# Optimization experiments

Measured on AMD Instinct MI355X. Metric: run time of the kernel, lower is better.

## Reference

```python
import jax, jax.numpy as jnp
import numpy as np
import math

B, T, WIDTH, NUM_HEADS, WINDOW = 2, 2048, 1024, 16, 1024
HEAD_DIM = WIDTH // NUM_HEADS
_MIN_LOGITS_VALUE = -1e30


def setup_inputs() -> dict:
    key = jax.random.key(0)
    k1, k2, k3, k4, k5 = jax.random.split(key, 5)
    std = math.sqrt(1.0 / WIDTH)
    x = jax.random.normal(k1, (B, T, WIDTH), dtype=jnp.float32)
    segment_pos = jnp.tile(jnp.arange(T, dtype=jnp.int32)[None, :], (B, 1))
    Wq = jax.random.normal(k2, (WIDTH, WIDTH), dtype=jnp.float32) * std
    Wk = jax.random.normal(k3, (HEAD_DIM, WIDTH), dtype=jnp.float32) * std
    Wv = jax.random.normal(k4, (HEAD_DIM, WIDTH), dtype=jnp.float32) * std
    Wf = jax.random.normal(k5, (WIDTH, WIDTH), dtype=jnp.float32) * std
    bf = jnp.zeros((WIDTH,), dtype=jnp.float32)
    return {"x": x, "segment_pos": segment_pos, "Wq": Wq, "Wk": Wk, "Wv": Wv, "Wf": Wf, "bf": bf}


def reference(x, segment_pos, Wq, Wk, Wv, Wf, bf):
    b, t, _ = x.shape
    # projections (torch Linear: y = x @ W.T)
    q = (x @ Wq.T).reshape(b, t, NUM_HEADS, HEAD_DIM)  # b t n h
    k = x @ Wk.T  # b s h  (single shared KV head, MQA)
    v = x @ Wv.T  # b s h
    scale = 1.0 / math.sqrt(HEAD_DIM)
    logits = jnp.einsum('btnh,bsh->bnts', q, k) * scale
    pos = jnp.arange(t)
    q_pos = pos[:, None]
    k_pos = pos[None, :]
    mask = (q_pos >= k_pos) & (q_pos <= k_pos + WINDOW)  # [t, t]
    masked = jnp.where(mask[None, None, :, :], logits, _MIN_LOGITS_VALUE)
    probs = jax.nn.softmax(masked.astype(jnp.float32), axis=-1).astype(logits.dtype)
    out = jnp.einsum('bnts,bsh->btnh', probs, v).reshape(b, t, WIDTH)
    return out @ Wf.T + bf
```

## Files before the change

### kernel.cpp

```cpp
#include <hip/hip_runtime.h>
#include <cstdint>
#include <cstddef>

#define BB      2
#define TT      2048
#define WID     1024
#define NH      16
#define HD      64
#define WIN     1024
#define MROWS   (BB*TT)
#define NQKV    1152
#define QSCL    0.18033688011112042f

typedef __attribute__((ext_vector_type(8))) short  short8;
typedef __attribute__((ext_vector_type(4))) float  floatx4;

__device__ __forceinline__ unsigned short f2bf(float f) {
  union { float f; unsigned int u; } v; v.f = f;
  unsigned int u = v.u;
  unsigned int r = (u + 0x7fffu + ((u >> 16) & 1u)) >> 16;
  return (unsigned short)r;
}

__device__ __forceinline__ float fast_exp2(float x) {
#if __has_builtin(__builtin_amdgcn_exp2f)
  return __builtin_amdgcn_exp2f(x);
#else
  return exp2f(x);
#endif
}

__device__ __forceinline__ unsigned int pk_bf16_trunc(float lo, float hi) {
  union { float f; unsigned int u; } a, b; a.f = lo; b.f = hi;
#if __has_builtin(__builtin_amdgcn_perm)
  return __builtin_amdgcn_perm(b.u, a.u, 0x07060302u);
#else
  return (b.u & 0xffff0000u) | (a.u >> 16);
#endif
}

__device__ __forceinline__ void gld_lds16(const void* g, void* l) {
  __builtin_amdgcn_global_load_lds(
      (const __attribute__((address_space(1))) unsigned int*)g,
      (__attribute__((address_space(3))) unsigned int*)l, 16, 0, 0);
}

__global__ __launch_bounds__(256) void convert_kernel(
    const float* __restrict__ x,  const float* __restrict__ wq,
    const float* __restrict__ wk, const float* __restrict__ wv,
    const float* __restrict__ wf,
    unsigned short* __restrict__ xb, unsigned short* __restrict__ wb,
    unsigned short* __restrict__ wfb)
{
  const int NX4 = (MROWS * WID) / 4;
  const int NQ4 = (WID * WID) / 4;
  const int NK4 = (HD * WID) / 4;
  const int NW4 = NQ4 + 2 * NK4;
  const int NF4 = (WID * WID) / 4;
  const int TOT = NX4 + NW4 + NF4;
  for (int i = blockIdx.x * blockDim.x + threadIdx.x; i < TOT;
       i += gridDim.x * blockDim.x) {
    float4 v4;
    unsigned short* dptr;
    if (i < NX4) {
      v4 = ((const float4*)x)[i];
      dptr = xb + (size_t)i * 4;
    } else if (i < NX4 + NW4) {
      int k = i - NX4;
      dptr = wb + (size_t)k * 4;
      if (k < NQ4)            v4 = ((const float4*)wq)[k];
      else if (k < NQ4 + NK4) v4 = ((const float4*)wk)[k - NQ4];
      else                    v4 = ((const float4*)wv)[k - NQ4 - NK4];
    } else {
      int k = i - NX4 - NW4;
      v4 = ((const float4*)wf)[k];
      dptr = wfb + (size_t)k * 4;
    }
    ushort4 o4 = make_ushort4(f2bf(v4.x), f2bf(v4.y), f2bf(v4.z), f2bf(v4.w));
    *(ushort4*)dptr = o4;
  }
}

__global__ __launch_bounds__(256) void gemm64(
    const unsigned short* __restrict__ A, const unsigned short* __restrict__ Bm,
    int M, int N, int K, int mode,
    float* __restrict__ C, const float* __restrict__ bias,
    unsigned short* __restrict__ qb, unsigned short* __restrict__ kb,
    unsigned short* __restrict__ vtb)
{
  __shared__ __align__(16) unsigned short As[2][64 * 64];
  __shared__ __align__(16) unsigned short Bs[2][128 * 64];

  const int tid  = threadIdx.x;
  const int m0   = blockIdx.x * 64;
  const int n0   = blockIdx.y * 128;
  const int w    = tid >> 6;
  const int lane = tid & 63;
  const int wr   = w >> 1;
  const int wc   = w & 1;
  const int quad = lane >> 4;
  const int l16  = lane & 15;

  const int rS  = tid >> 3;
  const int cS  = tid & 7;
  const int csS = (cS + rS) & 7;
  const unsigned short* gA0 = A  + (size_t)(m0 + rS) * K + csS * 8;
  const unsigned short* gA1 = gA0 + (size_t)32 * K;
  const unsigned short* gB0 = Bm + (size_t)(n0 + rS) * K + csS * 8;
  const unsigned short* gB1 = gB0 + (size_t)32 * K;
  const unsigned short* gB2 = gB0 + (size_t)64 * K;
  const unsigned short* gB3 = gB0 + (size_t)96 * K;
  const int wub = (tid & 192) * 16;

  floatx4 acc[2][4];
#pragma unroll
  for (int it = 0; it < 2; ++it)
#pragma unroll
    for (int jt = 0; jt < 4; ++jt)
      acc[it][jt] = (floatx4){0.f, 0.f, 0.f, 0.f};

  const int K64 = K >> 6;
  gld_lds16(gA0, (char*)As[0] + wub);
  gld_lds16(gA1, (char*)As[0] + 4096 + wub);
  gld_lds16(gB0, (char*)Bs[0] + wub);
  gld_lds16(gB1, (char*)Bs[0] + 4096 + wub);
  gld_lds16(gB2, (char*)Bs[0] + 8192 + wub);
  gld_lds16(gB3, (char*)Bs[0] + 12288 + wub);
  __syncthreads();

  for (int kt = 0; kt < K64; ++kt) {
    const int cur = kt & 1;
    if (kt + 1 < K64) {
      const int nxt = cur ^ 1;
      const int off = (kt + 1) * 64;
      gld_lds16(gA0 + off, (char*)As[nxt] + wub);
      gld_lds16(gA1 + off, (char*)As[nxt] + 4096 + wub);
      gld_lds16(gB0 + off, (char*)Bs[nxt] + wub);
      gld_lds16(gB1 + off, (char*)Bs[nxt] + 4096 + wub);
      gld_lds16(gB2 + off, (char*)Bs[nxt] + 8192 + wub);
      gld_lds16(gB3 + off, (char*)Bs[nxt] + 12288 + wub);
    }
    const unsigned short* as = As[cur];
    const unsigned short* bs = Bs[cur];
    short8 af[2][2], bfr[4][2];
#pragma unroll
    for (int it = 0; it < 2; ++it) {
      const int m = wr * 32 + it * 16 + l16;
#pragma unroll
      for (int ks = 0; ks < 2; ++ks)
        af[it][ks] = *(const short8*)(as + m * 64 + (((ks * 4 + quad) - m) & 7) * 8);
    }
#pragma unroll
    for (int jt = 0; jt < 4; ++jt) {
      const int n = wc * 64 + jt * 16 + l16;
#pragma unroll
      for (int ks = 0; ks < 2; ++ks)
        bfr[jt][ks] = *(const short8*)(bs + n * 64 + (((ks * 4 + quad) - n) & 7) * 8);
    }
#pragma unroll
    for (int ks = 0; ks < 2; ++ks)
#pragma unroll
      for (int it = 0; it < 2; ++it)
#pragma unroll
        for (int jt = 0; jt < 4; ++jt)
          acc[it][jt] = __builtin_amdgcn_mfma_f32_16x16x32_bf16(
              af[it][ks], bfr[jt][ks], acc[it][jt], 0, 0, 0);
    __syncthreads();
  }

  if (mode == 0) {
#pragma unroll
    for (int it = 0; it < 2; ++it) {
      const int gr = m0 + wr * 32 + it * 16 + quad * 4;
#pragma unroll
      for (int jt = 0; jt < 4; ++jt) {
        const int gc = n0 + wc * 64 + jt * 16 + l16;
        const float badd = bias[gc];
#pragma unroll
        for (int r = 0; r < 4; ++r)
          C[(size_t)(gr + r) * N + gc] = acc[it][jt][r] + badd;
      }
    }
  } else {
#pragma unroll
    for (int it = 0; it < 2; ++it) {
      const int gr = m0 + wr * 32 + it * 16 + quad * 4;
#pragma unroll
      for (int jt = 0; jt < 4; ++jt) {
        const int gc = n0 + wc * 64 + jt * 16 + l16;
        if (gc < WID) {
#pragma unroll
          for (int r = 0; r < 4; ++r)
            qb[(size_t)(gr + r) * WID + gc] = f2bf(acc[it][jt][r] * QSCL);
        } else if (gc < WID + HD) {
#pragma unroll
          for (int r = 0; r < 4; ++r)
            kb[(size_t)(gr + r) * HD + (gc - WID)] = f2bf(acc[it][jt][r]);
        } else {
          ushort4 o4 = make_ushort4(f2bf(acc[it][jt][0]), f2bf(acc[it][jt][1]),
                                    f2bf(acc[it][jt][2]), f2bf(acc[it][jt][3]));
          *(ushort4*)(vtb + (size_t)(gc - WID - HD) * MROWS + gr) = o4;
        }
      }
    }
  }
}

__global__ __launch_bounds__(256, 4) void attn_mfma(
    const unsigned short* __restrict__ qb, const unsigned short* __restrict__ kb,
    const unsigned short* __restrict__ vtb, unsigned short* __restrict__ attnb)
{
  __shared__ __align__(16) unsigned short smem[9472];

  const int tid  = threadIdx.x;
  const int w    = tid >> 6;
  const int g    = w >> 1;
  const int wh   = w & 1;
  const int lane = tid & 63;
  const int l16  = lane & 15;
  const int quad = lane >> 4;
  const int t0   = blockIdx.x * 32;
  const int h    = blockIdx.y * 2 + wh;
  const int b    = blockIdx.z;

  unsigned short* Psb = smem + w * 1280;

  short8 qf[2][2];
#pragma unroll
  for (int nt = 0; nt < 2; ++nt) {
    const unsigned short* qp =
        qb + (size_t)(b * TT + t0 + nt * 16 + l16) * WID + h * HD + quad * 8;
    qf[nt][0] = *(const short8*)qp;
    qf[nt][1] = *(const short8*)(qp + 32);
  }

  floatx4 Oacc[4][2];
#pragma unroll
  for (int mh = 0; mh < 4; ++mh)
#pragma unroll
    for (int nt = 0; nt < 2; ++nt)
      Oacc[mh][nt] = (floatx4){0.f, 0.f, 0.f, 0.f};
  float lq[2] = {0.f, 0.f};

  int s_begin = t0 - WIN; if (s_begin < 0) s_begin = 0;
  const int T = ((t0 + 32) - s_begin) >> 5;

  const unsigned short* kB = kb  + (size_t)(b * TT) * HD;

  for (int ta = g; ta < T; ta += 2) {
    const int s0 = s_begin + ta * 32;

    short8 kf[2][2];
#pragma unroll
    for (int mk = 0; mk < 2; ++mk) {
      const unsigned short* kp = kB + (size_t)(s0 + mk * 16 + l16) * HD + quad * 8;
      kf[mk][0] = *(const short8*)kp;
      kf[mk][1] = *(const short8*)(kp + 32);
    }

    floatx4 Sc[2][2];
#pragma unroll
    for (int mk = 0; mk < 2; ++mk)
#pragma unroll
      for (int nt = 0; nt < 2; ++nt)
        Sc[mk][nt] = (floatx4){0.f, 0.f, 0.f, 0.f};
#pragma unroll
    for (int mk = 0; mk < 2; ++mk)
#pragma unroll
      for (int nt = 0; nt < 2; ++nt)
#pragma unroll
        for (int k2 = 0; k2 < 2; ++k2)
          Sc[mk][nt] = __builtin_amdgcn_mfma_f32_16x16x32_bf16(
              kf[mk][k2], qf[nt][k2], Sc[mk][nt], 0, 0, 0);

    short8 vf[4];
#pragma unroll
    for (int mh = 0; mh < 4; ++mh)
      vf[mh] = *(const short8*)(vtb + (size_t)(mh * 16 + l16) * MROWS
                                + b * TT + s0 + quad * 8);

    const int mode = (s0 == t0) ? 2 : ((t0 >= WIN && s0 == t0 - WIN) ? 1 : 0);

#pragma unroll
    for (int nt = 0; nt < 2; ++nt) {
      const int t = t0 + nt * 16 + l16;
      float p[8], ps = 0.f;
#pragma unroll
      for (int mk = 0; mk < 2; ++mk)
#pragma unroll
        for (int r = 0; r < 4; ++r) {
          float v = Sc[mk][nt][r];
          if (mode) {
            const int s = s0 + mk * 16 + quad * 4 + r;
            const bool kill = (mode == 2) ? (s > t) : (s + WIN < t);
            if (kill) v = -1.0e5f;
          }
          const float e = fast_exp2(v);
          p[mk * 4 + r] = e; ps += e;
        }
      lq[nt] += ps;
      uint2 w0 = make_uint2(pk_bf16_trunc(p[0], p[1]), pk_bf16_trunc(p[2], p[3]));
      uint2 w1 = make_uint2(pk_bf16_trunc(p[4], p[5]), pk_bf16_trunc(p[6], p[7]));
      *(uint2*)(Psb + (nt * 16 + l16) * 40 + quad * 4)      = w0;
      *(uint2*)(Psb + (nt * 16 + l16) * 40 + 16 + quad * 4) = w1;
    }

    short8 pf0 = *(const short8*)(Psb + l16 * 40 + quad * 8);
    short8 pf1 = *(const short8*)(Psb + (16 + l16) * 40 + quad * 8);
#pragma unroll
    for (int mh = 0; mh < 4; ++mh) {
      Oacc[mh][0] = __builtin_amdgcn_mfma_f32_16x16x32_bf16(vf[mh], pf0, Oacc[mh][0], 0, 0, 0);
      Oacc[mh][1] = __builtin_amdgcn_mfma_f32_16x16x32_bf16(vf[mh], pf1, Oacc[mh][1], 0, 0, 0);
    }
  }

  lq[0] += __shfl_xor(lq[0], 16); lq[0] += __shfl_xor(lq[0], 32);
  lq[1] += __shfl_xor(lq[1], 16); lq[1] += __shfl_xor(lq[1], 32);

  __syncthreads();
  float* mrg = (float*)smem;
  float* ob  = mrg + wh * 2304 + lane * 36;
  if (g == 1) {
#pragma unroll
    for (int mh = 0; mh < 4; ++mh)
#pragma unroll
      for (int nt = 0; nt < 2; ++nt)
        *(floatx4*)(ob + mh * 8 + nt * 4) = Oacc[mh][nt];
    if (quad == 0) {
      mrg[4608 + wh * 32 + l16]      = lq[0];
      mrg[4608 + wh * 32 + 16 + l16] = lq[1];
    }
  }
  __syncthreads();
  if (g == 0) {
    lq[0] += mrg[4608 + wh * 32 + l16];
    lq[1] += mrg[4608 + wh * 32 + 16 + l16];
#pragma unroll
    for (int nt = 0; nt < 2; ++nt) {
      const float inv = 1.f / lq[nt];
      unsigned short* op = attnb + (size_t)(b * TT + t0 + nt * 16 + l16) * WID
                         + h * HD + quad * 4;
#pragma unroll
      for (int mh = 0; mh < 4; ++mh) {
        floatx4 o1 = *(const floatx4*)(ob + mh * 8 + nt * 4);
        ushort4 o4 = make_ushort4(f2bf((Oacc[mh][nt][0] + o1[0]) * inv),
                                  f2bf((Oacc[mh][nt][1] + o1[1]) * inv),
                                  f2bf((Oacc[mh][nt][2] + o1[2]) * inv),
                                  f2bf((Oacc[mh][nt][3] + o1[3]) * inv));
        *(ushort4*)(op + mh * 16) = o4;
      }
    }
  }
}

extern "C" void kernel_launch(void* const* d_in, const int* in_sizes, int n_in,
                              void* d_out, int out_size, void* d_ws, size_t ws_size,
                              hipStream_t stream) {
  const float* x   = (const float*)d_in[0];
  const float* wq  = (const float*)d_in[2];
  const float* wk  = (const float*)d_in[3];
  const float* wv  = (const float*)d_in[4];
  const float* wf  = (const float*)d_in[5];
  const float* bfp = (const float*)d_in[6];
  float* out = (float*)d_out;

  char* ws = (char*)d_ws;
  unsigned short* xb   = (unsigned short*)(ws + 0);
  unsigned short* wb   = (unsigned short*)(ws + 8388608);
  unsigned short* wfb  = (unsigned short*)(ws + 10747904);
  unsigned short* qbuf = (unsigned short*)(ws + 12845056);
  unsigned short* kbuf = (unsigned short*)(ws + 21233664);
  unsigned short* vtb  = (unsigned short*)(ws + 21757952);
  unsigned short* attnb = xb;

  hipLaunchKernelGGL(convert_kernel, dim3(1024), dim3(256), 0, stream,
                     x, wq, wk, wv, wf, xb, wb, wfb);
  hipLaunchKernelGGL(gemm64, dim3(MROWS / 64, NQKV / 128), dim3(256), 0, stream,
                     xb, wb, MROWS, NQKV, WID, 1,
                     (float*)nullptr, (const float*)nullptr, qbuf, kbuf, vtb);
  hipLaunchKernelGGL(attn_mfma, dim3(TT / 32, NH / 2, BB), dim3(256), 0, stream,
                     qbuf, kbuf, vtb, attnb);
  hipLaunchKernelGGL(gemm64, dim3(MROWS / 64, WID / 128), dim3(256), 0, stream,
                     attnb, wfb, MROWS, WID, WID, 0,
                     out, bfp, (unsigned short*)nullptr, (unsigned short*)nullptr,
                     (unsigned short*)nullptr);
}
```

Before: 182.8 us.

## Stage shared K tiles in LDS across four heads with 1024-thread attention blocks

The attention kernel now runs 16 waves per block: four key-tile groups times four heads. Each 128-row K chunk is loaded cooperatively into LDS once and reused by all four heads, and the next chunk is prefetched into registers while the current one is consumed. The partial outputs of the four key groups are merged through LDS in a sequential tree. This cuts redundant global K reads, but adds two block-wide barriers per iteration and idle waves when T is not a multiple of four. The larger blocks may also reduce occupancy.

Measured after the change: 340.4 us. 1.86x slower.

```diff
diff --git a/kernel.cpp b/kernel.cpp
--- a/kernel.cpp
+++ b/kernel.cpp
@@ -206,24 +206,24 @@
   }
 }
 
-__global__ __launch_bounds__(256, 4) void attn_mfma(
+__global__ __launch_bounds__(1024, 8) void attn_mfma(
     const unsigned short* __restrict__ qb, const unsigned short* __restrict__ kb,
     const unsigned short* __restrict__ vtb, unsigned short* __restrict__ attnb)
 {
-  __shared__ __align__(16) unsigned short smem[9472];
+  __shared__ __align__(16) unsigned short smem[30720];
 
   const int tid  = threadIdx.x;
   const int w    = tid >> 6;
-  const int g    = w >> 1;
-  const int wh   = w & 1;
+  const int g    = w >> 2;
+  const int wh   = w & 3;
   const int lane = tid & 63;
   const int l16  = lane & 15;
   const int quad = lane >> 4;
   const int t0   = blockIdx.x * 32;
-  const int h    = blockIdx.y * 2 + wh;
+  const int h    = blockIdx.y * 4 + wh;
   const int b    = blockIdx.z;
 
-  unsigned short* Psb = smem + w * 1280;
+  unsigned short* Psb = smem + 10240 + w * 1280;
 
   short8 qf[2][2];
 #pragma unroll
@@ -244,97 +244,158 @@
 
   int s_begin = t0 - WIN; if (s_begin < 0) s_begin = 0;
   const int T = ((t0 + 32) - s_begin) >> 5;
-
-  const unsigned short* kB = kb  + (size_t)(b * TT) * HD;
-
-  for (int ta = g; ta < T; ta += 2) {
-    const int s0 = s_begin + ta * 32;
-
-    short8 kf[2][2];
-#pragma unroll
-    for (int mk = 0; mk < 2; ++mk) {
-      const unsigned short* kp = kB + (size_t)(s0 + mk * 16 + l16) * HD + quad * 8;
-      kf[mk][0] = *(const short8*)kp;
-      kf[mk][1] = *(const short8*)(kp + 32);
-    }
-
-    floatx4 Sc[2][2];
-#pragma unroll
-    for (int mk = 0; mk < 2; ++mk)
+  const int I = (T + 3) >> 2;
+
+  const int gk  = tid >> 3;
+  const int kse = (tid & 7) * 8;
+  unsigned short* KsW = smem + (gk >> 5) * 2560 + (gk & 31) * 80 + kse;
+  const unsigned short* kbase = kb + (size_t)(b * TT) * HD;
+
+  int sK = s_begin;
+  int ck = sK + gk; if (ck > TT - 1) ck = TT - 1;
+  short8 kreg = *(const short8*)(kbase + (size_t)ck * HD + kse);
+
+  for (int i = 0; i < I; ++i) {
+    *(short8*)KsW = kreg;
+    __syncthreads();
+    if (i + 1 < I) {
+      sK += 128;
+      ck = sK + gk; if (ck > TT - 1) ck = TT - 1;
+      kreg = *(const short8*)(kbase + (size_t)ck * HD + kse);
+    }
+
+    const int ta = 4 * i + g;
+    if (ta < T) {
+      const int s0 = s_begin + ta * 32;
+      const unsigned short* ks = smem + g * 2560;
+
+      short8 kf[2][2];
+#pragma unroll
+      for (int mk = 0; mk < 2; ++mk)
+#pragma unroll
+        for (int k2 = 0; k2 < 2; ++k2)
+          kf[mk][k2] = *(const short8*)(ks + (mk * 16 + l16) * 80 + k2 * 32 + quad * 8);
+
+      floatx4 Sc[2][2];
+#pragma unroll
+      for (int mk = 0; mk < 2; ++mk)
+#pragma unroll
+        for (int nt = 0; nt < 2; ++nt)
+          Sc[mk][nt] = (floatx4){0.f, 0.f, 0.f, 0.f};
+#pragma unroll
+      for (int mk = 0; mk < 2; ++mk)
+#pragma unroll
+        for (int nt = 0; nt < 2; ++nt)
+#pragma unroll
+          for (int k2 = 0; k2 < 2; ++k2)
+            Sc[mk][nt] = __builtin_amdgcn_mfma_f32_16x16x32_bf16(
+                kf[mk][k2], qf[nt][k2], Sc[mk][nt], 0, 0, 0);
+
+      short8 vf[4];
+#pragma unroll
+      for (int mh = 0; mh < 4; ++mh)
+        vf[mh] = *(const short8*)(vtb + (size_t)(mh * 16 + l16) * MROWS
+                                  + b * TT + s0 + quad * 8);
+
+      const int mode = (s0 == t0) ? 2 : ((t0 >= WIN && s0 == t0 - WIN) ? 1 : 0);
+
+#pragma unroll
+      for (int nt = 0; nt < 2; ++nt) {
+        const int t = t0 + nt * 16 + l16;
+        float p[8], ps = 0.f;
+#pragma unroll
+        for (int mk = 0; mk < 2; ++mk)
+#pragma unroll
+          for (int r = 0; r < 4; ++r) {
+            float v = Sc[mk][nt][r];
+            if (mode) {
+              const int s = s0 + mk * 16 + quad * 4 + r;
+              const bool kill = (mode == 2) ? (s > t) : (s + WIN < t);
+              if (kill) v = -1.0e5f;
+            }
+            const float e = fast_exp2(v);
+            p[mk * 4 + r] = e; ps += e;
+          }
+        lq[nt] += ps;
+        uint2 w0 = make_uint2(pk_bf16_trunc(p[0], p[1]), pk_bf16_trunc(p[2], p[3]));
+        uint2 w1 = make_uint2(pk_bf16_trunc(p[4], p[5]), pk_bf16_trunc(p[6], p[7]));
+        *(uint2*)(Psb + (nt * 16 + l16) * 40 + quad * 4)      = w0;
+        *(uint2*)(Psb + (nt * 16 + l16) * 40 + 16 + quad * 4) = w1;
+      }
+
+      short8 pf0 = *(const short8*)(Psb + l16 * 40 + quad * 8);
+      short8 pf1 = *(const short8*)(Psb + (16 + l16) * 40 + quad * 8);
+#pragma unroll
+      for (int mh = 0; mh < 4; ++mh) {
+        Oacc[mh][0] = __builtin_amdgcn_mfma_f32_16x16x32_bf16(vf[mh], pf0, Oacc[mh][0], 0, 0, 0);
+        Oacc[mh][1] = __builtin_amdgcn_mfma_f32_16x16x32_bf16(vf[mh], pf1, Oacc[mh][1], 0, 0, 0);
+      }
+    }
+    __syncthreads();
+  }
+
+  float* row = (float*)smem + ((size_t)wh * 64 + lane) * 36;
+
+  if (g == 1) {
+#pragma unroll
+    for (int mh = 0; mh < 4; ++mh)
 #pragma unroll
       for (int nt = 0; nt < 2; ++nt)
-        Sc[mk][nt] = (floatx4){0.f, 0.f, 0.f, 0.f};
-#pragma unroll
-    for (int mk = 0; mk < 2; ++mk)
+        *(floatx4*)(row + mh * 8 + nt * 4) = Oacc[mh][nt];
+    row[32] = lq[0]; row[33] = lq[1];
+  }
+  __syncthreads();
+  if (g == 0) {
+#pragma unroll
+    for (int mh = 0; mh < 4; ++mh)
+#pragma unroll
+      for (int nt = 0; nt < 2; ++nt) {
+        floatx4 o1 = *(const floatx4*)(row + mh * 8 + nt * 4);
+        Oacc[mh][nt] += o1;
+      }
+    lq[0] += row[32]; lq[1] += row[33];
+  }
+  __syncthreads();
+  if (g == 3) {
+#pragma unroll
+    for (int mh = 0; mh < 4; ++mh)
 #pragma unroll
       for (int nt = 0; nt < 2; ++nt)
-#pragma unroll
-        for (int k2 = 0; k2 < 2; ++k2)
-          Sc[mk][nt] = __builtin_amdgcn_mfma_f32_16x16x32_bf16(
-              kf[mk][k2], qf[nt][k2], Sc[mk][nt], 0, 0, 0);
-
-    short8 vf[4];
-#pragma unroll
-    for (int mh = 0; mh < 4; ++mh)
-      vf[mh] = *(const short8*)(vtb + (size_t)(mh * 16 + l16) * MROWS
-                                + b * TT + s0 + quad * 8);
-
-    const int mode = (s0 == t0) ? 2 : ((t0 >= WIN && s0 == t0 - WIN) ? 1 : 0);
-
-#pragma unroll
-    for (int nt = 0; nt < 2; ++nt) {
-      const int t = t0 + nt * 16 + l16;
-      float p[8], ps = 0.f;
-#pragma unroll
-      for (int mk = 0; mk < 2; ++mk)
-#pragma unroll
-        for (int r = 0; r < 4; ++r) {
-          float v = Sc[mk][nt][r];
-          if (mode) {
-            const int s = s0 + mk * 16 + quad * 4 + r;
-            const bool kill = (mode == 2) ? (s > t) : (s + WIN < t);
-            if (kill) v = -1.0e5f;
-          }
-          const float e = fast_exp2(v);
-          p[mk * 4 + r] = e; ps += e;
-        }
-      lq[nt] += ps;
-      uint2 w0 = make_uint2(pk_bf16_trunc(p[0], p[1]), pk_bf16_trunc(p[2], p[3]));
-      uint2 w1 = make_uint2(pk_bf16_trunc(p[4], p[5]), pk_bf16_trunc(p[6], p[7]));
-      *(uint2*)(Psb + (nt * 16 + l16) * 40 + quad * 4)      = w0;
-      *(uint2*)(Psb + (nt * 16 + l16) * 40 + 16 + quad * 4) = w1;
-    }
-
-    short8 pf0 = *(const short8*)(Psb + l16 * 40 + quad * 8);
-    short8 pf1 = *(const short8*)(Psb + (16 + l16) * 40 + quad * 8);
-#pragma unroll
-    for (int mh = 0; mh < 4; ++mh) {
-      Oacc[mh][0] = __builtin_amdgcn_mfma_f32_16x16x32_bf16(vf[mh], pf0, Oacc[mh][0], 0, 0, 0);
-      Oacc[mh][1] = __builtin_amdgcn_mfma_f32_16x16x32_bf16(vf[mh], pf1, Oacc[mh][1], 0, 0, 0);
-    }
-  }
-
-  lq[0] += __shfl_xor(lq[0], 16); lq[0] += __shfl_xor(lq[0], 32);
-  lq[1] += __shfl_xor(lq[1], 16); lq[1] += __shfl_xor(lq[1], 32);
-
-  __syncthreads();
-  float* mrg = (float*)smem;
-  float* ob  = mrg + wh * 2304 + lane * 36;
-  if (g == 1) {
+        *(floatx4*)(row + mh * 8 + nt * 4) = Oacc[mh][nt];
+    row[32] = lq[0]; row[33] = lq[1];
+  }
+  __syncthreads();
+  if (g == 2) {
+#pragma unroll
+    for (int mh = 0; mh < 4; ++mh)
+#pragma unroll
+      for (int nt = 0; nt < 2; ++nt) {
+        floatx4 o1 = *(const floatx4*)(row + mh * 8 + nt * 4);
+        Oacc[mh][nt] += o1;
+      }
+    lq[0] += row[32]; lq[1] += row[33];
+  }
+  __syncthreads();
+  if (g == 2) {
 #pragma unroll
     for (int mh = 0; mh < 4; ++mh)
 #pragma unroll
       for (int nt = 0; nt < 2; ++nt)
-        *(floatx4*)(ob + mh * 8 + nt * 4) = Oacc[mh][nt];
-    if (quad == 0) {
-      mrg[4608 + wh * 32 + l16]      = lq[0];
-      mrg[4608 + wh * 32 + 16 + l16] = lq[1];
-    }
+        *(floatx4*)(row + mh * 8 + nt * 4) = Oacc[mh][nt];
+    row[32] = lq[0]; row[33] = lq[1];
   }
   __syncthreads();
   if (g == 0) {
-    lq[0] += mrg[4608 + wh * 32 + l16];
-    lq[1] += mrg[4608 + wh * 32 + 16 + l16];
+#pragma unroll
+    for (int mh = 0; mh < 4; ++mh)
+#pragma unroll
+      for (int nt = 0; nt < 2; ++nt) {
+        floatx4 o1 = *(const floatx4*)(row + mh * 8 + nt * 4);
+        Oacc[mh][nt] += o1;
+      }
+    lq[0] += row[32]; lq[1] += row[33];
+    lq[0] += __shfl_xor(lq[0], 16); lq[0] += __shfl_xor(lq[0], 32);
+    lq[1] += __shfl_xor(lq[1], 16); lq[1] += __shfl_xor(lq[1], 32);
 #pragma unroll
     for (int nt = 0; nt < 2; ++nt) {
       const float inv = 1.f / lq[nt];
@@ -342,11 +403,10 @@
                          + h * HD + quad * 4;
 #pragma unroll
       for (int mh = 0; mh < 4; ++mh) {
-        floatx4 o1 = *(const floatx4*)(ob + mh * 8 + nt * 4);
-        ushort4 o4 = make_ushort4(f2bf((Oacc[mh][nt][0] + o1[0]) * inv),
-                                  f2bf((Oacc[mh][nt][1] + o1[1]) * inv),
-                                  f2bf((Oacc[mh][nt][2] + o1[2]) * inv),
-                                  f2bf((Oacc[mh][nt][3] + o1[3]) * inv));
+        ushort4 o4 = make_ushort4(f2bf(Oacc[mh][nt][0] * inv),
+                                  f2bf(Oacc[mh][nt][1] * inv),
+                                  f2bf(Oacc[mh][nt][2] * inv),
+                                  f2bf(Oacc[mh][nt][3] * inv));
         *(ushort4*)(op + mh * 16) = o4;
       }
     }
@@ -378,7 +438,7 @@
   hipLaunchKernelGGL(gemm64, dim3(MROWS / 64, NQKV / 128), dim3(256), 0, stream,
                      xb, wb, MROWS, NQKV, WID, 1,
                      (float*)nullptr, (const float*)nullptr, qbuf, kbuf, vtb);
-  hipLaunchKernelGGL(attn_mfma, dim3(TT / 32, NH / 2, BB), dim3(256), 0, stream,
+  hipLaunchKernelGGL(attn_mfma, dim3(TT / 32, NH / 4, BB), dim3(1024), 0, stream,
                      qbuf, kbuf, vtb, attnb);
   hipLaunchKernelGGL(gemm64, dim3(MROWS / 64, WID / 128), dim3(256), 0, stream,
                      attnb, wfb, MROWS, WID, WID, 0,
```

## Stage K tiles through double-buffered shared memory with register prefetch

Applied to the files above, without the earlier changes.

The attention kernel now loads each 64-key K tile cooperatively into a double-buffered LDS region, prefetching the next tile into registers while the current one is consumed. Each warp group then reads its 32-key K fragments from shared memory instead of issuing its own global loads. The cost is a __syncthreads per iteration, a larger LDS footprint that may reduce occupancy, and a reworked merge buffer layout that stores row sums alongside the partial outputs.

Result: faster. 161.4 us (-11.7%).

```diff
diff --git a/kernel.cpp b/kernel.cpp
--- a/kernel.cpp
+++ b/kernel.cpp
@@ -210,7 +210,7 @@
     const unsigned short* __restrict__ qb, const unsigned short* __restrict__ kb,
     const unsigned short* __restrict__ vtb, unsigned short* __restrict__ attnb)
 {
-  __shared__ __align__(16) unsigned short smem[9472];
+  __shared__ __align__(16) unsigned short smem[14336];
 
   const int tid  = threadIdx.x;
   const int w    = tid >> 6;
@@ -223,7 +223,7 @@
   const int h    = blockIdx.y * 2 + wh;
   const int b    = blockIdx.z;
 
-  unsigned short* Psb = smem + w * 1280;
+  unsigned short* Psb = smem + 9216 + w * 1280;
 
   short8 qf[2][2];
 #pragma unroll
@@ -244,73 +244,98 @@
 
   int s_begin = t0 - WIN; if (s_begin < 0) s_begin = 0;
   const int T = ((t0 + 32) - s_begin) >> 5;
-
-  const unsigned short* kB = kb  + (size_t)(b * TT) * HD;
-
-  for (int ta = g; ta < T; ta += 2) {
-    const int s0 = s_begin + ta * 32;
-
-    short8 kf[2][2];
-#pragma unroll
-    for (int mk = 0; mk < 2; ++mk) {
-      const unsigned short* kp = kB + (size_t)(s0 + mk * 16 + l16) * HD + quad * 8;
-      kf[mk][0] = *(const short8*)kp;
-      kf[mk][1] = *(const short8*)(kp + 32);
-    }
-
-    floatx4 Sc[2][2];
-#pragma unroll
-    for (int mk = 0; mk < 2; ++mk)
-#pragma unroll
-      for (int nt = 0; nt < 2; ++nt)
-        Sc[mk][nt] = (floatx4){0.f, 0.f, 0.f, 0.f};
-#pragma unroll
-    for (int mk = 0; mk < 2; ++mk)
-#pragma unroll
-      for (int nt = 0; nt < 2; ++nt)
+  const int I = (T + 1) >> 1;
+
+  const int key0 = tid >> 3,          hs0 = (tid & 7) * 8;
+  const int key1 = (tid + 256) >> 3,  hs1 = hs0;
+  const unsigned short* kbase = kb + (size_t)(b * TT) * HD;
+
+  int sr = s_begin;
+  int c0 = sr + key0; if (c0 > TT - 1) c0 = TT - 1;
+  int c1 = sr + key1; if (c1 > TT - 1) c1 = TT - 1;
+  short8 kreg0 = *(const short8*)(kbase + (size_t)c0 * HD + hs0);
+  short8 kreg1 = *(const short8*)(kbase + (size_t)c1 * HD + hs1);
+
+  for (int i = 0; i < I; ++i) {
+    const int buf = i & 1;
+    unsigned short* kd = smem + buf * 4608;
+    *(short8*)(kd + (key0 >> 5) * 2304 + (key0 & 31) * 72 + hs0) = kreg0;
+    *(short8*)(kd + (key1 >> 5) * 2304 + (key1 & 31) * 72 + hs1) = kreg1;
+    __syncthreads();
+    if (i + 1 < I) {
+      sr += 64;
+      c0 = sr + key0; if (c0 > TT - 1) c0 = TT - 1;
+      c1 = sr + key1; if (c1 > TT - 1) c1 = TT - 1;
+      kreg0 = *(const short8*)(kbase + (size_t)c0 * HD + hs0);
+      kreg1 = *(const short8*)(kbase + (size_t)c1 * HD + hs1);
+    }
+
+    const int ta = 2 * i + g;
+    if (ta < T) {
+      const int s0 = s_begin + ta * 32;
+      const unsigned short* ks = smem + buf * 4608 + g * 2304;
+
+      short8 kf[2][2];
+#pragma unroll
+      for (int mk = 0; mk < 2; ++mk)
 #pragma unroll
         for (int k2 = 0; k2 < 2; ++k2)
-          Sc[mk][nt] = __builtin_amdgcn_mfma_f32_16x16x32_bf16(
-              kf[mk][k2], qf[nt][k2], Sc[mk][nt], 0, 0, 0);
-
-    short8 vf[4];
-#pragma unroll
-    for (int mh = 0; mh < 4; ++mh)
-      vf[mh] = *(const short8*)(vtb + (size_t)(mh * 16 + l16) * MROWS
-                                + b * TT + s0 + quad * 8);
-
-    const int mode = (s0 == t0) ? 2 : ((t0 >= WIN && s0 == t0 - WIN) ? 1 : 0);
-
-#pragma unroll
-    for (int nt = 0; nt < 2; ++nt) {
-      const int t = t0 + nt * 16 + l16;
-      float p[8], ps = 0.f;
+          kf[mk][k2] = *(const short8*)(ks + (mk * 16 + l16) * 72 + k2 * 32 + quad * 8);
+
+      floatx4 Sc[2][2];
 #pragma unroll
       for (int mk = 0; mk < 2; ++mk)
 #pragma unroll
-        for (int r = 0; r < 4; ++r) {
-          float v = Sc[mk][nt][r];
-          if (mode) {
-            const int s = s0 + mk * 16 + quad * 4 + r;
-            const bool kill = (mode == 2) ? (s > t) : (s + WIN < t);
-            if (kill) v = -1.0e5f;
+        for (int nt = 0; nt < 2; ++nt)
+          Sc[mk][nt] = (floatx4){0.f, 0.f, 0.f, 0.f};
+#pragma unroll
+      for (int mk = 0; mk < 2; ++mk)
+#pragma unroll
+        for (int nt = 0; nt < 2; ++nt)
+#pragma unroll
+          for (int k2 = 0; k2 < 2; ++k2)
+            Sc[mk][nt] = __builtin_amdgcn_mfma_f32_16x16x32_bf16(
+                kf[mk][k2], qf[nt][k2], Sc[mk][nt], 0, 0, 0);
+
+      short8 vf[4];
+#pragma unroll
+      for (int mh = 0; mh < 4; ++mh)
+        vf[mh] = *(const short8*)(vtb + (size_t)(mh * 16 + l16) * MROWS
+                                  + b * TT + s0 + quad * 8);
+
+      const int mode = (s0 == t0) ? 2 : ((t0 >= WIN && s0 == t0 - WIN) ? 1 : 0);
+
+#pragma unroll
+      for (int nt = 0; nt < 2; ++nt) {
+        const int t = t0 + nt * 16 + l16;
+        float p[8], ps = 0.f;
+#pragma unroll
+        for (int mk = 0; mk < 2; ++mk)
+#pragma unroll
+          for (int r = 0; r < 4; ++r) {
+            float v = Sc[mk][nt][r];
+            if (mode) {
+              const int s = s0 + mk * 16 + quad * 4 + r;
+              const bool kill = (mode == 2) ? (s > t) : (s + WIN < t);
+              if (kill) v = -1.0e5f;
+            }
+            const float e = fast_exp2(v);
+            p[mk * 4 + r] = e; ps += e;
           }
-          const float e = fast_exp2(v);
-          p[mk * 4 + r] = e; ps += e;
-        }
-      lq[nt] += ps;
-      uint2 w0 = make_uint2(pk_bf16_trunc(p[0], p[1]), pk_bf16_trunc(p[2], p[3]));
-      uint2 w1 = make_uint2(pk_bf16_trunc(p[4], p[5]), pk_bf16_trunc(p[6], p[7]));
-      *(uint2*)(Psb + (nt * 16 + l16) * 40 + quad * 4)      = w0;
-      *(uint2*)(Psb + (nt * 16 + l16) * 40 + 16 + quad * 4) = w1;
-    }
-
-    short8 pf0 = *(const short8*)(Psb + l16 * 40 + quad * 8);
-    short8 pf1 = *(const short8*)(Psb + (16 + l16) * 40 + quad * 8);
-#pragma unroll
-    for (int mh = 0; mh < 4; ++mh) {
-      Oacc[mh][0] = __builtin_amdgcn_mfma_f32_16x16x32_bf16(vf[mh], pf0, Oacc[mh][0], 0, 0, 0);
-      Oacc[mh][1] = __builtin_amdgcn_mfma_f32_16x16x32_bf16(vf[mh], pf1, Oacc[mh][1], 0, 0, 0);
+        lq[nt] += ps;
+        uint2 w0 = make_uint2(pk_bf16_trunc(p[0], p[1]), pk_bf16_trunc(p[2], p[3]));
+        uint2 w1 = make_uint2(pk_bf16_trunc(p[4], p[5]), pk_bf16_trunc(p[6], p[7]));
+        *(uint2*)(Psb + (nt * 16 + l16) * 40 + quad * 4)      = w0;
+        *(uint2*)(Psb + (nt * 16 + l16) * 40 + 16 + quad * 4) = w1;
+      }
+
+      short8 pf0 = *(const short8*)(Psb + l16 * 40 + quad * 8);
+      short8 pf1 = *(const short8*)(Psb + (16 + l16) * 40 + quad * 8);
+#pragma unroll
+      for (int mh = 0; mh < 4; ++mh) {
+        Oacc[mh][0] = __builtin_amdgcn_mfma_f32_16x16x32_bf16(vf[mh], pf0, Oacc[mh][0], 0, 0, 0);
+        Oacc[mh][1] = __builtin_amdgcn_mfma_f32_16x16x32_bf16(vf[mh], pf1, Oacc[mh][1], 0, 0, 0);
+      }
     }
   }
 
@@ -319,22 +344,18 @@
 
   __syncthreads();
   float* mrg = (float*)smem;
-  float* ob  = mrg + wh * 2304 + lane * 36;
+  float* ob  = mrg + ((size_t)wh * 64 + lane) * 36;
   if (g == 1) {
 #pragma unroll
     for (int mh = 0; mh < 4; ++mh)
 #pragma unroll
       for (int nt = 0; nt < 2; ++nt)
         *(floatx4*)(ob + mh * 8 + nt * 4) = Oacc[mh][nt];
-    if (quad == 0) {
-      mrg[4608 + wh * 32 + l16]      = lq[0];
-      mrg[4608 + wh * 32 + 16 + l16] = lq[1];
-    }
+    ob[32] = lq[0]; ob[33] = lq[1];
   }
   __syncthreads();
   if (g == 0) {
-    lq[0] += mrg[4608 + wh * 32 + l16];
-    lq[1] += mrg[4608 + wh * 32 + 16 + l16];
+    lq[0] += ob[32]; lq[1] += ob[33];
 #pragma unroll
     for (int nt = 0; nt < 2; ++nt) {
       const float inv = 1.f / lq[nt];
```
